# Optimization experiments

Measured on AMD Instinct MI355X. Metric: run time of the kernel, lower is better.

## Reference

```python
import jax, jax.numpy as jnp
import numpy as np

EPS = 1e-6

def ln_fwd(x, gamma, beta):
    # gamma/beta broadcast shape [1,H,1,D]
    mu = x.mean(axis=-1, keepdims=True)
    var = ((x - mu) ** 2).mean(axis=-1, keepdims=True)
    x_hat = (x - mu) / jnp.sqrt(var + EPS)
    return gamma * x_hat + beta

def ln_fused_l2_bwd(x, residual, pred, gamma, beta):
    # grad wrt x of || (gamma*ln(x)+beta) + residual - pred ||^2 (fused form)
    mu = x.mean(axis=-1, keepdims=True)
    var = ((x - mu) ** 2).mean(axis=-1, keepdims=True)
    std = jnp.sqrt(var + EPS)
    x_hat = (x - mu) / std
    y = gamma * x_hat + beta + residual
    grad_output = 2.0 * (y - pred)
    gxh = grad_output * gamma
    z = (gxh - gxh.mean(axis=-1, keepdims=True)
         - x_hat * (gxh * x_hat).mean(axis=-1, keepdims=True)) / std
    return z

def _combine(a, b):
    # a precedes b in sequence; recurrence x[t] = g[t]*x[t-1] + u[t]
    ga, ua = a
    gb, ub = b
    return (ga * gb, gb * ua + ub)

def setup_inputs() -> dict:
    key = jax.random.key(0)
    ks = jax.random.split(key, 8)
    B, H, L, D = 1, 16, 2048, 64
    q = jax.random.normal(ks[0], (B, H, L, D), dtype=jnp.float32)
    k = jax.random.normal(ks[1], (B, H, L, D), dtype=jnp.float32)
    v = jax.random.normal(ks[2], (B, H, L, D), dtype=jnp.float32)
    gate = jax.random.uniform(ks[3], (B, H, L), dtype=jnp.float32)
    eta = jax.random.uniform(ks[4], (B, H, L), dtype=jnp.float32) * 0.1
    W0 = jax.random.normal(ks[5], (H, D, D), dtype=jnp.float32) / jnp.sqrt(jnp.float32(D))
    gamma = jnp.ones((H, 1, D), dtype=jnp.float32)
    beta = jnp.zeros((H, 1, D), dtype=jnp.float32)
    return {"q": q, "k": k, "v": v, "gate": gate, "eta": eta,
            "W0": W0, "gamma": gamma, "beta": beta}

def reference(q, k, v, gate, eta, W0, gamma, beta):
    # q,k,v: [B,H,L,D]; gate,eta: [B,H,L]; W0: [H,D,D]; gamma,beta: [H,1,D]
    g = gamma[None]          # [1,H,1,D]
    b = beta[None]
    # inner-loop TTT gradient at initial fast weights W0
    Z1 = jnp.einsum('bhld,hde->bhle', k, W0)                  # [B,H,L,D]
    grad_l = ln_fused_l2_bwd(Z1, k, v, g, b)                  # [B,H,L,D]
    # per-token fast-weight update: -eta[t] * outer(k[t], grad_l[t])
    token = -eta[..., None, None] * (k[..., :, None] * grad_l[..., None, :])  # [B,H,L,D,D]
    gates = gate[..., None, None]                             # [B,H,L,1,1]
    # gated linear recurrence W[t] = gate[t]*W[t-1] + token[t] via associative scan
    gc, uc = jax.lax.associative_scan(_combine, (gates, token), axis=2)
    W = uc + gc * W0[None, :, None]                           # [B,H,L,D,D]
    # readout with post-LN and residual
    Zq = jnp.einsum('bhld,bhlde->bhle', q, W)                 # [B,H,L,D]
    out = ln_fwd(Zq, g, b) + q
    return out
```

## Files before the change

### kernel.cpp

```cpp
#include <hip/hip_runtime.h>
#include <hip/hip_bf16.h>
#include <math.h>


#define H 16
#define L 2048
#define D 64
#define C 64
#define NC 32

typedef short s8v __attribute__((ext_vector_type(8)));
typedef short s4v __attribute__((ext_vector_type(4)));
typedef float f4v __attribute__((ext_vector_type(4)));

__device__ inline unsigned short f2bf(float x) {
  unsigned u = __float_as_uint(x);
  return (unsigned short)((u + 0x7fffu + ((u >> 16) & 1u)) >> 16);
}
__device__ inline float bf2f(unsigned short s) { return __uint_as_float(((unsigned)s) << 16); }

__device__ inline int swz(int row, int colByte) { return row * 128 + (colByte ^ ((row & 7) << 4)); }

__device__ inline s8v ld8(const short* base, int row, int colByte) {
  return *(const s8v*)((const char*)base + swz(row, colByte));
}
__device__ inline void st4(short* base, int row, int colByte, s4v v) {
  *(s4v*)((char*)base + swz(row, colByte)) = v;
}
__device__ inline void st1(short* base, int row, int colByte, unsigned short v) {
  *(short*)((char*)base + swz(row, colByte)) = (short)v;
}

__device__ inline void red16(float& x) {
  x += __shfl_xor(x, 1, 64);
  x += __shfl_xor(x, 2, 64);
  x += __shfl_xor(x, 4, 64);
  x += __shfl_xor(x, 8, 64);
}

__device__ inline f4v MM(s8v a, s8v b, f4v c) {
  return __builtin_amdgcn_mfma_f32_16x16x32_bf16(a, b, c, 0, 0, 0);
}

__device__ inline f4v MM3(s8v ah, s8v al, s8v bh, s8v bl, f4v c) {
  c = MM(ah, bh, c);
  c = MM(ah, bl, c);
  c = MM(al, bh, c);
  return c;
}

__global__ __launch_bounds__(256) void k_chunk(
    const float4* __restrict__ Q4, const float4* __restrict__ K4,
    const float* __restrict__ Kg, const float* __restrict__ Vg,
    const float* __restrict__ gate, const float* __restrict__ eta,
    const float4* __restrict__ W04, const float* __restrict__ gamma,
    const float* __restrict__ beta,
    float* __restrict__ Ut, float* __restrict__ Pg, float* __restrict__ Out)
{
  __shared__ __align__(16) short Qhi[4096];
  __shared__ __align__(16) short Qlo[4096];
  __shared__ __align__(16) short Khi[4096];
  __shared__ __align__(16) short Klo[4096];
  __shared__ __align__(16) short KtH[4096];
  __shared__ __align__(16) short KtL[4096];
  __shared__ __align__(16) short W0h[4096];
  __shared__ __align__(16) short W0l[4096];
  __shared__ float cl[64], wj[64];

  int tid = threadIdx.x;
  int h = blockIdx.x >> 5, c = blockIdx.x & 31;
  int rowb = h * L + c * C;

  if (tid < 64) {
    float x = logf(fmaxf(gate[rowb + tid], 1e-37f));
    #pragma unroll
    for (int off = 1; off < 64; off <<= 1) {
      float n = __shfl_up(x, off, 64);
      if (tid >= off) x += n;
    }
    cl[tid] = x;
    float c63 = __shfl(x, 63, 64);
    wj[tid] = expf(c63 - x);
    Pg[rowb + tid] = expf(x);
  }
  __syncthreads();

  for (int idx = tid; idx < 1024; idx += 256) {
    int row = idx >> 4, g4 = idx & 15, cb = g4 * 8;
    float4 kv = K4[(rowb + row) * 16 + g4];
    float ke[4] = {kv.x, kv.y, kv.z, kv.w};
    float wr = wj[row];
    s4v khv, klv;
    #pragma unroll
    for (int e = 0; e < 4; ++e) {
      unsigned short hb = f2bf(ke[e]);
      khv[e] = (short)hb;
      klv[e] = (short)f2bf(ke[e] - bf2f(hb));
      float wk = ke[e] * wr;
      unsigned short wh = f2bf(wk);
      st1(KtH, 4 * g4 + e, 2 * row, wh);
      st1(KtL, 4 * g4 + e, 2 * row, f2bf(wk - bf2f(wh)));
    }
    st4(Khi, row, cb, khv);
    st4(Klo, row, cb, klv);
    float4 qv = Q4[(rowb + row) * 16 + g4];
    float qe[4] = {qv.x, qv.y, qv.z, qv.w};
    s4v qh, ql;
    #pragma unroll
    for (int e = 0; e < 4; ++e) {
      unsigned short hb = f2bf(qe[e]);
      qh[e] = (short)hb;
      ql[e] = (short)f2bf(qe[e] - bf2f(hb));
    }
    st4(Qhi, row, cb, qh);
    st4(Qlo, row, cb, ql);
    float4 wv = W04[h * 1024 + idx];
    float we[4] = {wv.x, wv.y, wv.z, wv.w};
    #pragma unroll
    for (int e = 0; e < 4; ++e) {
      unsigned short hb = f2bf(we[e]);
      st1(W0h, 4 * g4 + e, 2 * row, hb);
      st1(W0l, 4 * g4 + e, 2 * row, f2bf(we[e] - bf2f(hb)));
    }
  }
  __syncthreads();

  int R = tid >> 6, l = tid & 63, g = l >> 4, c16 = l & 15;
  int arow = 16 * R + c16;
  int kb0 = 16 * g, kb1 = 64 + 16 * g;

  s8v aQh0 = ld8(Qhi, arow, kb0), aQh1 = ld8(Qhi, arow, kb1);
  s8v aQl0 = ld8(Qlo, arow, kb0), aQl1 = ld8(Qlo, arow, kb1);
  f4v accS[4];
  #pragma unroll
  for (int ct = 0; ct < 4; ++ct) {
    int br = 16 * ct + c16;
    f4v a = {0.f, 0.f, 0.f, 0.f};
    a = MM3(aQh0, aQl0, ld8(Khi, br, kb0), ld8(Klo, br, kb0), a);
    a = MM3(aQh1, aQl1, ld8(Khi, br, kb1), ld8(Klo, br, kb1), a);
    accS[ct] = a;
  }

  s8v aKh0 = ld8(Khi, arow, kb0), aKh1 = ld8(Khi, arow, kb1);
  s8v aKl0 = ld8(Klo, arow, kb0), aKl1 = ld8(Klo, arow, kb1);
  f4v accZ[4];
  #pragma unroll
  for (int ct = 0; ct < 4; ++ct) {
    int br = 16 * ct + c16;
    f4v a = {0.f, 0.f, 0.f, 0.f};
    a = MM3(aKh0, aKl0, ld8(W0h, br, kb0), ld8(W0l, br, kb0), a);
    a = MM3(aKh1, aKl1, ld8(W0h, br, kb1), ld8(W0l, br, kb1), a);
    accZ[ct] = a;
  }

  float ga[4], be[4];
  #pragma unroll
  for (int ct = 0; ct < 4; ++ct) {
    ga[ct] = gamma[h * 64 + 16 * ct + c16];
    be[ct] = beta[h * 64 + 16 * ct + c16];
  }
  float gtreg[4][4];
  #pragma unroll
  for (int r = 0; r < 4; ++r) {
    int jr = 16 * R + 4 * g + r;
    int grow = (rowb + jr) * 64;
    float kk[4], vv[4];
    #pragma unroll
    for (int ct = 0; ct < 4; ++ct) {
      kk[ct] = Kg[grow + 16 * ct + c16];
      vv[ct] = Vg[grow + 16 * ct + c16];
    }
    float s1 = accZ[0][r] + accZ[1][r] + accZ[2][r] + accZ[3][r];
    red16(s1);
    float mu = s1 * (1.f / 64.f);
    float dv[4], s2 = 0.f;
    #pragma unroll
    for (int ct = 0; ct < 4; ++ct) { dv[ct] = accZ[ct][r] - mu; s2 += dv[ct] * dv[ct]; }
    red16(s2);
    float rstd = rsqrtf(s2 * (1.f / 64.f) + 1e-6f);
    float xh[4], gxh[4], t1 = 0.f, t2 = 0.f;
    #pragma unroll
    for (int ct = 0; ct < 4; ++ct) {
      xh[ct] = dv[ct] * rstd;
      float go = 2.f * (fmaf(ga[ct], xh[ct], be[ct]) + kk[ct] - vv[ct]);
      gxh[ct] = go * ga[ct];
      t1 += gxh[ct];
      t2 += gxh[ct] * xh[ct];
    }
    red16(t1);
    red16(t2);
    float m1 = t1 * (1.f / 64.f), m2 = t2 * (1.f / 64.f);
    float er = eta[rowb + jr];
    #pragma unroll
    for (int ct = 0; ct < 4; ++ct)
      gtreg[r][ct] = -er * (gxh[ct] - m1 - xh[ct] * m2) * rstd;
  }
  __syncthreads();

  #pragma unroll
  for (int r = 0; r < 4; ++r) {
    int jr = 16 * R + 4 * g + r;
    #pragma unroll
    for (int ct = 0; ct < 4; ++ct) {
      float gtv = gtreg[r][ct];
      unsigned short hb = f2bf(gtv);
      st1(W0h, 16 * ct + c16, 2 * jr, hb);
      st1(W0l, 16 * ct + c16, 2 * jr, f2bf(gtv - bf2f(hb)));
    }
  }
  float cli[4];
  #pragma unroll
  for (int r = 0; r < 4; ++r) cli[r] = cl[16 * R + 4 * g + r];
  #pragma unroll
  for (int ct = 0; ct < 4; ++ct) {
    int j = 16 * ct + c16;
    float clj = cl[j];
    #pragma unroll
    for (int r = 0; r < 4; ++r) {
      int i = 16 * R + 4 * g + r;
      float s = (j <= i) ? accS[ct][r] * expf(cli[r] - clj) : 0.f;
      unsigned short hb = f2bf(s);
      st1(Qhi, i, 2 * j, hb);
      st1(Qlo, i, 2 * j, f2bf(s - bf2f(hb)));
    }
  }
  __syncthreads();

  s8v aSh0 = ld8(Qhi, arow, kb0), aSh1 = ld8(Qhi, arow, kb1);
  s8v aSl0 = ld8(Qlo, arow, kb0), aSl1 = ld8(Qlo, arow, kb1);
  #pragma unroll
  for (int ct = 0; ct < 4; ++ct) {
    int br = 16 * ct + c16;
    f4v a = {0.f, 0.f, 0.f, 0.f};
    a = MM3(aSh0, aSl0, ld8(W0h, br, kb0), ld8(W0l, br, kb0), a);
    a = MM3(aSh1, aSl1, ld8(W0h, br, kb1), ld8(W0l, br, kb1), a);
    #pragma unroll
    for (int r = 0; r < 4; ++r)
      Out[(rowb + 16 * R + 4 * g + r) * 64 + 16 * ct + c16] = a[r];
  }

  float* ub = Ut + (h * NC + c) * 4096;
  s8v aGh0 = ld8(W0h, arow, kb0), aGh1 = ld8(W0h, arow, kb1);
  s8v aGl0 = ld8(W0l, arow, kb0), aGl1 = ld8(W0l, arow, kb1);
  #pragma unroll
  for (int ct = 0; ct < 4; ++ct) {
    int br = 16 * ct + c16;
    f4v a = {0.f, 0.f, 0.f, 0.f};
    a = MM3(aGh0, aGl0, ld8(KtH, br, kb0), ld8(KtL, br, kb0), a);
    a = MM3(aGh1, aGl1, ld8(KtH, br, kb1), ld8(KtL, br, kb1), a);
    #pragma unroll
    for (int r = 0; r < 4; ++r)
      ub[(16 * R + 4 * g + r) * 64 + 16 * ct + c16] = a[r];
  }
}

__global__ __launch_bounds__(256) void k_scan(
    const float* __restrict__ W0, const float* __restrict__ Ut,
    const float* __restrict__ Pg, float* __restrict__ Wpt)
{
  int t = blockIdx.x * 256 + threadIdx.x;
  int h = t >> 12;
  int idx = t & 4095;
  int erow = idx >> 6, d = idx & 63;
  float w = W0[h * 4096 + d * 64 + erow];
  #pragma unroll
  for (int c2 = 0; c2 < NC; ++c2) {
    int off = (h * NC + c2) * 4096 + idx;
    Wpt[off] = w;
    w = fmaf(Pg[h * L + c2 * 64 + 63], w, Ut[off]);
  }
}

__global__ __launch_bounds__(256) void k_out(
    const float4* __restrict__ Q4, const float* __restrict__ Qg,
    const float4* __restrict__ Wpt4, const float* __restrict__ Pg,
    const float* __restrict__ gamma, const float* __restrict__ beta,
    float* __restrict__ Out)
{
  __shared__ __align__(16) short Qhi[4096];
  __shared__ __align__(16) short Qlo[4096];
  __shared__ __align__(16) short Whi[4096];
  __shared__ __align__(16) short Wlo[4096];
  int tid = threadIdx.x;
  int h = blockIdx.x >> 5, c = blockIdx.x & 31;
  int rowb = h * L + c * C;
  for (int idx = tid; idx < 1024; idx += 256) {
    int row = idx >> 4, g4 = idx & 15, cb = g4 * 8;
    float4 qv = Q4[(rowb + row) * 16 + g4];
    float qe[4] = {qv.x, qv.y, qv.z, qv.w};
    s4v qh, ql;
    #pragma unroll
    for (int e = 0; e < 4; ++e) {
      unsigned short hb = f2bf(qe[e]);
      qh[e] = (short)hb;
      ql[e] = (short)f2bf(qe[e] - bf2f(hb));
    }
    st4(Qhi, row, cb, qh);
    st4(Qlo, row, cb, ql);
    float4 wv = Wpt4[(h * NC + c) * 1024 + idx];
    float we[4] = {wv.x, wv.y, wv.z, wv.w};
    s4v wh, wl;
    #pragma unroll
    for (int e = 0; e < 4; ++e) {
      unsigned short hb = f2bf(we[e]);
      wh[e] = (short)hb;
      wl[e] = (short)f2bf(we[e] - bf2f(hb));
    }
    st4(Whi, row, cb, wh);
    st4(Wlo, row, cb, wl);
  }
  __syncthreads();

  int R = tid >> 6, l = tid & 63, g = l >> 4, c16 = l & 15;
  int arow = 16 * R + c16;
  int kb0 = 16 * g, kb1 = 64 + 16 * g;
  s8v ah0 = ld8(Qhi, arow, kb0), ah1 = ld8(Qhi, arow, kb1);
  s8v al0 = ld8(Qlo, arow, kb0), al1 = ld8(Qlo, arow, kb1);
  f4v acc[4];
  #pragma unroll
  for (int ct = 0; ct < 4; ++ct) {
    int br = 16 * ct + c16;
    f4v a = {0.f, 0.f, 0.f, 0.f};
    a = MM3(ah0, al0, ld8(Whi, br, kb0), ld8(Wlo, br, kb0), a);
    a = MM3(ah1, al1, ld8(Whi, br, kb1), ld8(Wlo, br, kb1), a);
    acc[ct] = a;
  }
  float ga[4], be[4];
  #pragma unroll
  for (int ct = 0; ct < 4; ++ct) {
    ga[ct] = gamma[h * 64 + 16 * ct + c16];
    be[ct] = beta[h * 64 + 16 * ct + c16];
  }
  #pragma unroll
  for (int r = 0; r < 4; ++r) {
    int row = rowb + 16 * R + 4 * g + r;
    float pr = Pg[row];
    float zq[4];
    #pragma unroll
    for (int ct = 0; ct < 4; ++ct)
      zq[ct] = fmaf(pr, acc[ct][r], Out[row * 64 + 16 * ct + c16]);
    float s1 = zq[0] + zq[1] + zq[2] + zq[3];
    red16(s1);
    float mu = s1 * (1.f / 64.f);
    float dv[4], s2 = 0.f;
    #pragma unroll
    for (int ct = 0; ct < 4; ++ct) { dv[ct] = zq[ct] - mu; s2 += dv[ct] * dv[ct]; }
    red16(s2);
    float rstd = rsqrtf(s2 * (1.f / 64.f) + 1e-6f);
    #pragma unroll
    for (int ct = 0; ct < 4; ++ct) {
      float o = fmaf(ga[ct], dv[ct] * rstd, be[ct]) + Qg[row * 64 + 16 * ct + c16];
      Out[row * 64 + 16 * ct + c16] = o;
    }
  }
}

extern "C" void kernel_launch(void* const* d_in, const int* in_sizes, int n_in,
                              void* d_out, int out_size, void* d_ws, size_t ws_size,
                              hipStream_t stream) {
  const float* q     = (const float*)d_in[0];
  const float* k     = (const float*)d_in[1];
  const float* v     = (const float*)d_in[2];
  const float* gate  = (const float*)d_in[3];
  const float* eta   = (const float*)d_in[4];
  const float* W0    = (const float*)d_in[5];
  const float* gamma = (const float*)d_in[6];
  const float* beta  = (const float*)d_in[7];
  float* out = (float*)d_out;
  float* ws  = (float*)d_ws;

  float* Pg  = ws;
  float* Ut  = ws + 32768;
  float* Wpt = ws + 32768 + 2097152;

  k_chunk<<<H * NC, 256, 0, stream>>>(
      (const float4*)q, (const float4*)k, k, v, gate, eta,
      (const float4*)W0, gamma, beta, Ut, Pg, out);
  k_scan<<<256, 256, 0, stream>>>(W0, Ut, Pg, Wpt);
  k_out<<<H * NC, 256, 0, stream>>>(
      (const float4*)q, q, (const float4*)Wpt, Pg, gamma, beta, out);
}
```

Measured before the change: 32.47 us.

## Load Q fragments straight into registers, prefetch K/V/eta early, drop Q LDS staging

Q is now read from global memory directly into MFMA A-operand registers and split to bf16 hi/lo there, which removes the Qhi/Qlo shared buffers in both kernels. The S matrix reuses the K buffers instead. K, V, eta, Pg and the residual loads are issued at kernel start so their latency overlaps the prefix scan and LDS staging, and the gate scan is merged into the same barrier phase. LDS stores are widened to 2-element and 4-element writes, and launch bounds request 2 blocks per CU. The trade-off is more registers held live across the early phase, which could spill under the tighter launch bound.

```diff
diff --git a/kernel.cpp b/kernel.cpp
--- a/kernel.cpp
+++ b/kernel.cpp
@@ -27,6 +27,9 @@
 __device__ inline void st4(short* base, int row, int colByte, s4v v) {
   *(s4v*)((char*)base + swz(row, colByte)) = v;
 }
+__device__ inline void st2(short* base, int row, int colByte, unsigned v) {
+  *(unsigned*)((char*)base + swz(row, colByte)) = v;
+}
 __device__ inline void st1(short* base, int row, int colByte, unsigned short v) {
   *(short*)((char*)base + swz(row, colByte)) = (short)v;
 }
@@ -49,7 +52,7 @@
   return c;
 }
 
-__global__ __launch_bounds__(256) void k_chunk(
+__global__ __launch_bounds__(256, 2) void k_chunk(
     const float4* __restrict__ Q4, const float4* __restrict__ K4,
     const float* __restrict__ Kg, const float* __restrict__ Vg,
     const float* __restrict__ gate, const float* __restrict__ eta,
@@ -57,8 +60,6 @@
     const float* __restrict__ beta,
     float* __restrict__ Ut, float* __restrict__ Pg, float* __restrict__ Out)
 {
-  __shared__ __align__(16) short Qhi[4096];
-  __shared__ __align__(16) short Qlo[4096];
   __shared__ __align__(16) short Khi[4096];
   __shared__ __align__(16) short Klo[4096];
   __shared__ __align__(16) short KtH[4096];
@@ -70,67 +71,89 @@
   int tid = threadIdx.x;
   int h = blockIdx.x >> 5, c = blockIdx.x & 31;
   int rowb = h * L + c * C;
-
-  if (tid < 64) {
-    float x = logf(fmaxf(gate[rowb + tid], 1e-37f));
-    #pragma unroll
-    for (int off = 1; off < 64; off <<= 1) {
-      float n = __shfl_up(x, off, 64);
-      if (tid >= off) x += n;
-    }
-    cl[tid] = x;
-    float c63 = __shfl(x, 63, 64);
-    wj[tid] = expf(c63 - x);
-    Pg[rowb + tid] = expf(x);
-  }
-  __syncthreads();
-
-  for (int idx = tid; idx < 1024; idx += 256) {
-    int row = idx >> 4, g4 = idx & 15, cb = g4 * 8;
-    float4 kv = K4[(rowb + row) * 16 + g4];
-    float ke[4] = {kv.x, kv.y, kv.z, kv.w};
-    float wr = wj[row];
-    s4v khv, klv;
-    #pragma unroll
-    for (int e = 0; e < 4; ++e) {
-      unsigned short hb = f2bf(ke[e]);
-      khv[e] = (short)hb;
-      klv[e] = (short)f2bf(ke[e] - bf2f(hb));
-      float wk = ke[e] * wr;
-      unsigned short wh = f2bf(wk);
-      st1(KtH, 4 * g4 + e, 2 * row, wh);
-      st1(KtL, 4 * g4 + e, 2 * row, f2bf(wk - bf2f(wh)));
-    }
-    st4(Khi, row, cb, khv);
-    st4(Klo, row, cb, klv);
-    float4 qv = Q4[(rowb + row) * 16 + g4];
-    float qe[4] = {qv.x, qv.y, qv.z, qv.w};
-    s4v qh, ql;
-    #pragma unroll
-    for (int e = 0; e < 4; ++e) {
-      unsigned short hb = f2bf(qe[e]);
-      qh[e] = (short)hb;
-      ql[e] = (short)f2bf(qe[e] - bf2f(hb));
-    }
-    st4(Qhi, row, cb, qh);
-    st4(Qlo, row, cb, ql);
-    float4 wv = W04[h * 1024 + idx];
-    float we[4] = {wv.x, wv.y, wv.z, wv.w};
-    #pragma unroll
-    for (int e = 0; e < 4; ++e) {
-      unsigned short hb = f2bf(we[e]);
-      st1(W0h, 4 * g4 + e, 2 * row, hb);
-      st1(W0l, 4 * g4 + e, 2 * row, f2bf(we[e] - bf2f(hb)));
-    }
-  }
-  __syncthreads();
-
   int R = tid >> 6, l = tid & 63, g = l >> 4, c16 = l & 15;
   int arow = 16 * R + c16;
   int kb0 = 16 * g, kb1 = 64 + 16 * g;
 
-  s8v aQh0 = ld8(Qhi, arow, kb0), aQh1 = ld8(Qhi, arow, kb1);
-  s8v aQl0 = ld8(Qlo, arow, kb0), aQl1 = ld8(Qlo, arow, kb1);
+  const float4* qp = Q4 + (size_t)(rowb + arow) * 16;
+  float4 qA0 = qp[2 * g], qA1 = qp[2 * g + 1], qA2 = qp[8 + 2 * g], qA3 = qp[8 + 2 * g + 1];
+  float kk[4][4], vv[4][4], er[4];
+  #pragma unroll
+  for (int r = 0; r < 4; ++r) {
+    int jr = 16 * R + 4 * g + r;
+    const float* kp = Kg + (size_t)(rowb + jr) * 64 + c16;
+    const float* vp = Vg + (size_t)(rowb + jr) * 64 + c16;
+    #pragma unroll
+    for (int ct = 0; ct < 4; ++ct) {
+      kk[r][ct] = kp[16 * ct];
+      vv[r][ct] = vp[16 * ct];
+    }
+    er[r] = eta[rowb + jr];
+  }
+
+  {
+    float x = logf(fmaxf(gate[rowb + l], 1e-37f));
+    #pragma unroll
+    for (int off = 1; off < 64; off <<= 1) {
+      float n = __shfl_up(x, off, 64);
+      if (l >= off) x += n;
+    }
+    cl[l] = x;
+    float c63 = __shfl(x, 63, 64);
+    wj[l] = expf(c63 - x);
+    if (R == 0) Pg[rowb + l] = expf(x);
+  }
+
+  #pragma unroll
+  for (int it = 0; it < 2; ++it) {
+    int idx = tid + it * 256;
+    int rp = idx >> 4, g4 = idx & 15;
+    int j0 = 2 * rp, j1 = j0 + 1;
+    float4 k0 = K4[(size_t)(rowb + j0) * 16 + g4];
+    float4 k1 = K4[(size_t)(rowb + j1) * 16 + g4];
+    float4 w0 = W04[(size_t)h * 1024 + j0 * 16 + g4];
+    float4 w1 = W04[(size_t)h * 1024 + j1 * 16 + g4];
+    float w0j = wj[j0], w1j = wj[j1];
+    float ke0[4] = {k0.x, k0.y, k0.z, k0.w};
+    float ke1[4] = {k1.x, k1.y, k1.z, k1.w};
+    float we0[4] = {w0.x, w0.y, w0.z, w0.w};
+    float we1[4] = {w1.x, w1.y, w1.z, w1.w};
+    s4v kh0, kl0, kh1, kl1;
+    #pragma unroll
+    for (int e = 0; e < 4; ++e) {
+      unsigned short hb0 = f2bf(ke0[e]);
+      kh0[e] = (short)hb0; kl0[e] = (short)f2bf(ke0[e] - bf2f(hb0));
+      unsigned short hb1 = f2bf(ke1[e]);
+      kh1[e] = (short)hb1; kl1[e] = (short)f2bf(ke1[e] - bf2f(hb1));
+      int dr = 4 * g4 + e;
+      float wk0 = ke0[e] * w0j, wk1 = ke1[e] * w1j;
+      unsigned short th0 = f2bf(wk0), th1 = f2bf(wk1);
+      st2(KtH, dr, 2 * j0, (unsigned)th0 | ((unsigned)th1 << 16));
+      st2(KtL, dr, 2 * j0,
+          (unsigned)f2bf(wk0 - bf2f(th0)) | ((unsigned)f2bf(wk1 - bf2f(th1)) << 16));
+      unsigned short wh0 = f2bf(we0[e]), wh1 = f2bf(we1[e]);
+      st2(W0h, dr, 2 * j0, (unsigned)wh0 | ((unsigned)wh1 << 16));
+      st2(W0l, dr, 2 * j0,
+          (unsigned)f2bf(we0[e] - bf2f(wh0)) | ((unsigned)f2bf(we1[e] - bf2f(wh1)) << 16));
+    }
+    st4(Khi, j0, 8 * g4, kh0); st4(Klo, j0, 8 * g4, kl0);
+    st4(Khi, j1, 8 * g4, kh1); st4(Klo, j1, 8 * g4, kl1);
+  }
+
+  s8v aQh0, aQl0, aQh1, aQl1;
+  {
+    float q0[8] = {qA0.x, qA0.y, qA0.z, qA0.w, qA1.x, qA1.y, qA1.z, qA1.w};
+    float q1[8] = {qA2.x, qA2.y, qA2.z, qA2.w, qA3.x, qA3.y, qA3.z, qA3.w};
+    #pragma unroll
+    for (int e = 0; e < 8; ++e) {
+      unsigned short hb = f2bf(q0[e]);
+      aQh0[e] = (short)hb; aQl0[e] = (short)f2bf(q0[e] - bf2f(hb));
+      unsigned short hb1 = f2bf(q1[e]);
+      aQh1[e] = (short)hb1; aQl1[e] = (short)f2bf(q1[e] - bf2f(hb1));
+    }
+  }
+  __syncthreads();
+
   f4v accS[4];
   #pragma unroll
   for (int ct = 0; ct < 4; ++ct) {
@@ -162,14 +185,6 @@
   float gtreg[4][4];
   #pragma unroll
   for (int r = 0; r < 4; ++r) {
-    int jr = 16 * R + 4 * g + r;
-    int grow = (rowb + jr) * 64;
-    float kk[4], vv[4];
-    #pragma unroll
-    for (int ct = 0; ct < 4; ++ct) {
-      kk[ct] = Kg[grow + 16 * ct + c16];
-      vv[ct] = Vg[grow + 16 * ct + c16];
-    }
     float s1 = accZ[0][r] + accZ[1][r] + accZ[2][r] + accZ[3][r];
     red16(s1);
     float mu = s1 * (1.f / 64.f);
@@ -182,7 +197,7 @@
     #pragma unroll
     for (int ct = 0; ct < 4; ++ct) {
       xh[ct] = dv[ct] * rstd;
-      float go = 2.f * (fmaf(ga[ct], xh[ct], be[ct]) + kk[ct] - vv[ct]);
+      float go = 2.f * (fmaf(ga[ct], xh[ct], be[ct]) + kk[r][ct] - vv[r][ct]);
       gxh[ct] = go * ga[ct];
       t1 += gxh[ct];
       t2 += gxh[ct] * xh[ct];
@@ -190,23 +205,23 @@
     red16(t1);
     red16(t2);
     float m1 = t1 * (1.f / 64.f), m2 = t2 * (1.f / 64.f);
-    float er = eta[rowb + jr];
     #pragma unroll
     for (int ct = 0; ct < 4; ++ct)
-      gtreg[r][ct] = -er * (gxh[ct] - m1 - xh[ct] * m2) * rstd;
+      gtreg[r][ct] = -er[r] * (gxh[ct] - m1 - xh[ct] * m2) * rstd;
   }
   __syncthreads();
 
   #pragma unroll
-  for (int r = 0; r < 4; ++r) {
-    int jr = 16 * R + 4 * g + r;
-    #pragma unroll
-    for (int ct = 0; ct < 4; ++ct) {
-      float gtv = gtreg[r][ct];
-      unsigned short hb = f2bf(gtv);
-      st1(W0h, 16 * ct + c16, 2 * jr, hb);
-      st1(W0l, 16 * ct + c16, 2 * jr, f2bf(gtv - bf2f(hb)));
-    }
+  for (int ct = 0; ct < 4; ++ct) {
+    s4v gh, gl;
+    #pragma unroll
+    for (int r = 0; r < 4; ++r) {
+      unsigned short hb = f2bf(gtreg[r][ct]);
+      gh[r] = (short)hb;
+      gl[r] = (short)f2bf(gtreg[r][ct] - bf2f(hb));
+    }
+    st4(W0h, 16 * ct + c16, 2 * (16 * R + 4 * g), gh);
+    st4(W0l, 16 * ct + c16, 2 * (16 * R + 4 * g), gl);
   }
   float cli[4];
   #pragma unroll
@@ -220,14 +235,14 @@
       int i = 16 * R + 4 * g + r;
       float s = (j <= i) ? accS[ct][r] * expf(cli[r] - clj) : 0.f;
       unsigned short hb = f2bf(s);
-      st1(Qhi, i, 2 * j, hb);
-      st1(Qlo, i, 2 * j, f2bf(s - bf2f(hb)));
+      st1(Khi, i, 2 * j, hb);
+      st1(Klo, i, 2 * j, f2bf(s - bf2f(hb)));
     }
   }
   __syncthreads();
 
-  s8v aSh0 = ld8(Qhi, arow, kb0), aSh1 = ld8(Qhi, arow, kb1);
-  s8v aSl0 = ld8(Qlo, arow, kb0), aSl1 = ld8(Qlo, arow, kb1);
+  s8v aSh0 = ld8(Khi, arow, kb0), aSh1 = ld8(Khi, arow, kb1);
+  s8v aSl0 = ld8(Klo, arow, kb0), aSl1 = ld8(Klo, arow, kb1);
   #pragma unroll
   for (int ct = 0; ct < 4; ++ct) {
     int br = 16 * ct + c16;
@@ -236,10 +251,10 @@
     a = MM3(aSh1, aSl1, ld8(W0h, br, kb1), ld8(W0l, br, kb1), a);
     #pragma unroll
     for (int r = 0; r < 4; ++r)
-      Out[(rowb + 16 * R + 4 * g + r) * 64 + 16 * ct + c16] = a[r];
-  }
-
-  float* ub = Ut + (h * NC + c) * 4096;
+      Out[(size_t)(rowb + 16 * R + 4 * g + r) * 64 + 16 * ct + c16] = a[r];
+  }
+
+  float* ub = Ut + (size_t)(h * NC + c) * 4096;
   s8v aGh0 = ld8(W0h, arow, kb0), aGh1 = ld8(W0h, arow, kb1);
   s8v aGl0 = ld8(W0l, arow, kb0), aGl1 = ld8(W0l, arow, kb1);
   #pragma unroll
@@ -271,33 +286,38 @@
   }
 }
 
-__global__ __launch_bounds__(256) void k_out(
+__global__ __launch_bounds__(256, 2) void k_out(
     const float4* __restrict__ Q4, const float* __restrict__ Qg,
     const float4* __restrict__ Wpt4, const float* __restrict__ Pg,
     const float* __restrict__ gamma, const float* __restrict__ beta,
     float* __restrict__ Out)
 {
-  __shared__ __align__(16) short Qhi[4096];
-  __shared__ __align__(16) short Qlo[4096];
   __shared__ __align__(16) short Whi[4096];
   __shared__ __align__(16) short Wlo[4096];
   int tid = threadIdx.x;
   int h = blockIdx.x >> 5, c = blockIdx.x & 31;
   int rowb = h * L + c * C;
+  int R = tid >> 6, l = tid & 63, g = l >> 4, c16 = l & 15;
+  int arow = 16 * R + c16;
+  int kb0 = 16 * g, kb1 = 64 + 16 * g;
+
+  const float4* qp = Q4 + (size_t)(rowb + arow) * 16;
+  float4 qA0 = qp[2 * g], qA1 = qp[2 * g + 1], qA2 = qp[8 + 2 * g], qA3 = qp[8 + 2 * g + 1];
+  float io[4][4], qres[4][4], pr[4];
+  #pragma unroll
+  for (int r = 0; r < 4; ++r) {
+    int row = rowb + 16 * R + 4 * g + r;
+    pr[r] = Pg[row];
+    #pragma unroll
+    for (int ct = 0; ct < 4; ++ct) {
+      io[r][ct] = Out[(size_t)row * 64 + 16 * ct + c16];
+      qres[r][ct] = Qg[(size_t)row * 64 + 16 * ct + c16];
+    }
+  }
+
   for (int idx = tid; idx < 1024; idx += 256) {
-    int row = idx >> 4, g4 = idx & 15, cb = g4 * 8;
-    float4 qv = Q4[(rowb + row) * 16 + g4];
-    float qe[4] = {qv.x, qv.y, qv.z, qv.w};
-    s4v qh, ql;
-    #pragma unroll
-    for (int e = 0; e < 4; ++e) {
-      unsigned short hb = f2bf(qe[e]);
-      qh[e] = (short)hb;
-      ql[e] = (short)f2bf(qe[e] - bf2f(hb));
-    }
-    st4(Qhi, row, cb, qh);
-    st4(Qlo, row, cb, ql);
-    float4 wv = Wpt4[(h * NC + c) * 1024 + idx];
+    int row = idx >> 4, g4 = idx & 15;
+    float4 wv = Wpt4[(size_t)(h * NC + c) * 1024 + idx];
     float we[4] = {wv.x, wv.y, wv.z, wv.w};
     s4v wh, wl;
     #pragma unroll
@@ -306,16 +326,24 @@
       wh[e] = (short)hb;
       wl[e] = (short)f2bf(we[e] - bf2f(hb));
     }
-    st4(Whi, row, cb, wh);
-    st4(Wlo, row, cb, wl);
+    st4(Whi, row, 8 * g4, wh);
+    st4(Wlo, row, 8 * g4, wl);
+  }
+
+  s8v ah0, al0, ah1, al1;
+  {
+    float q0[8] = {qA0.x, qA0.y, qA0.z, qA0.w, qA1.x, qA1.y, qA1.z, qA1.w};
+    float q1[8] = {qA2.x, qA2.y, qA2.z, qA2.w, qA3.x, qA3.y, qA3.z, qA3.w};
+    #pragma unroll
+    for (int e = 0; e < 8; ++e) {
+      unsigned short hb = f2bf(q0[e]);
+      ah0[e] = (short)hb; al0[e] = (short)f2bf(q0[e] - bf2f(hb));
+      unsigned short hb1 = f2bf(q1[e]);
+      ah1[e] = (short)hb1; al1[e] = (short)f2bf(q1[e] - bf2f(hb1));
+    }
   }
   __syncthreads();
 
-  int R = tid >> 6, l = tid & 63, g = l >> 4, c16 = l & 15;
-  int arow = 16 * R + c16;
-  int kb0 = 16 * g, kb1 = 64 + 16 * g;
-  s8v ah0 = ld8(Qhi, arow, kb0), ah1 = ld8(Qhi, arow, kb1);
-  s8v al0 = ld8(Qlo, arow, kb0), al1 = ld8(Qlo, arow, kb1);
   f4v acc[4];
   #pragma unroll
   for (int ct = 0; ct < 4; ++ct) {
@@ -334,11 +362,10 @@
   #pragma unroll
   for (int r = 0; r < 4; ++r) {
     int row = rowb + 16 * R + 4 * g + r;
-    float pr = Pg[row];
     float zq[4];
     #pragma unroll
     for (int ct = 0; ct < 4; ++ct)
-      zq[ct] = fmaf(pr, acc[ct][r], Out[row * 64 + 16 * ct + c16]);
+      zq[ct] = fmaf(pr[r], acc[ct][r], io[r][ct]);
     float s1 = zq[0] + zq[1] + zq[2] + zq[3];
     red16(s1);
     float mu = s1 * (1.f / 64.f);
@@ -349,8 +376,8 @@
     float rstd = rsqrtf(s2 * (1.f / 64.f) + 1e-6f);
     #pragma unroll
     for (int ct = 0; ct < 4; ++ct) {
-      float o = fmaf(ga[ct], dv[ct] * rstd, be[ct]) + Qg[row * 64 + 16 * ct + c16];
-      Out[row * 64 + 16 * ct + c16] = o;
+      float o = fmaf(ga[ct], dv[ct] * rstd, be[ct]) + qres[r][ct];
+      Out[(size_t)row * 64 + 16 * ct + c16] = o;
     }
   }
 }
```

Measured after the change: 31.87 us. Within noise of the previous version (-1.8%).
